# Optimization experiments

Hardware: AMD Instinct MI355X
Metric: run time of the kernel (lower is better)

Reference implementation:

```python
import jax, jax.numpy as jnp
import numpy as np

D_MODEL, H, KV, HD = 2048, 32, 8, 64  # head_dim = 64, RoPE half-dim = 32
B, L = 2, 2048
EPS = 1e-06


def apply_rope(t, cos, sin):
    # t: [b,l,h,hd]; cos/sin: [1,l,1,hd//2] (broadcast over batch and heads)
    dim = t.shape[-1] // 2
    cos = cos[..., :dim]
    sin = sin[..., :dim]
    x1, x2 = t[..., :dim], t[..., dim:]
    return jnp.concatenate([x1 * cos - x2 * sin, x2 * cos + x1 * sin], axis=-1)


def setup_inputs() -> dict:
    key = jax.random.key(0)
    ks = jax.random.split(key, 5)
    x = jax.random.normal(ks[0], (B, L, D_MODEL), dtype=jnp.float32)
    # true rotary tables, theta=10000
    half = HD // 2
    inv_freq = 1.0 / (10000.0 ** (jnp.arange(half, dtype=jnp.float32) / half))
    ang = jnp.arange(L, dtype=jnp.float32)[:, None] * inv_freq[None, :]  # [L, half]
    cos = jnp.cos(ang)[None, :, None, :]  # [1,L,1,half]
    sin = jnp.sin(ang)[None, :, None, :]
    s = 0.02
    Wq = jax.random.normal(ks[1], (D_MODEL, D_MODEL), dtype=jnp.float32) * s
    Wk = jax.random.normal(ks[2], (D_MODEL, KV * HD), dtype=jnp.float32) * s
    Wv = jax.random.normal(ks[3], (D_MODEL, KV * HD), dtype=jnp.float32) * s
    Wo = jax.random.normal(ks[4], (D_MODEL, D_MODEL), dtype=jnp.float32) * s
    return {"x": x, "cos": cos, "sin": sin, "Wq": Wq, "Wk": Wk, "Wv": Wv, "Wo": Wo}


def reference(x, cos, sin, Wq, Wk, Wv, Wo):
    b, l, _ = x.shape
    q = (x @ Wq).reshape(b, l, H, HD)
    k = (x @ Wk).reshape(b, l, KV, HD)
    v = (x @ Wv).reshape(b, l, KV, HD)
    q = apply_rope(q, cos, sin)
    k = apply_rope(k, cos[:, :, :KV, :], sin[:, :, :KV, :])
    # QK RMS-norm (qk_norm=True path), done in fp32
    q32 = q.astype(jnp.float32)
    k32 = k.astype(jnp.float32)
    q = (q32 * jax.lax.rsqrt(jnp.mean(jnp.square(q32), axis=-1, keepdims=True) + EPS)).astype(q.dtype)
    k = (k32 * jax.lax.rsqrt(jnp.mean(jnp.square(k32), axis=-1, keepdims=True) + EPS)).astype(k.dtype)
    # GQA: repeat KV heads to match Q heads
    g = H // KV
    k = jnp.repeat(k, g, axis=2)
    v = jnp.repeat(v, g, axis=2)
    scale = jax.lax.rsqrt(jnp.float32(HD))
    scores = jnp.einsum('blhd,bmhd->bhlm', q, k) * scale  # [b,H,L,L]
    causal = jnp.tril(jnp.ones((l, l), dtype=jnp.bool_))[None, None]
    scores = jnp.where(causal, scores, jnp.full_like(scores, -10000.0))
    attn = jax.nn.softmax(scores.astype(jnp.float32), axis=-1).astype(v.dtype)
    out = jnp.einsum('bhql,blhd->bqhd', attn, v).reshape(b, l, D_MODEL)
    return out @ Wo
```

## Files before the change

### kernel.cpp

```cpp
#include <hip/hip_runtime.h>
#include <hip/hip_bf16.h>
#include <cstdint>
#include <cstddef>

#define D_MODEL 2048
#define NH 32
#define NKV 8
#define HD 64
#define BB 2
#define LL 2048
#define EPS 1e-6f
#define MM (BB * LL)
#define QS 3072
#define KO 2048
#define VO 2560
#define QSCALE 0.18033688f

typedef __hip_bfloat16 bf16;
typedef short bf16x8 __attribute__((ext_vector_type(8)));
typedef short s16x4 __attribute__((ext_vector_type(4)));
typedef float f32x4 __attribute__((ext_vector_type(4)));

__device__ inline float4 ld_bf4u(const unsigned short* p) {
  const ushort4 u = *(const ushort4*)p;
  float4 r;
  r.x = __uint_as_float(((unsigned)u.x) << 16);
  r.y = __uint_as_float(((unsigned)u.y) << 16);
  r.z = __uint_as_float(((unsigned)u.z) << 16);
  r.w = __uint_as_float(((unsigned)u.w) << 16);
  return r;
}
__device__ inline float4 ld4_rt(const void* p, size_t i, bool f32) {
  if (f32) return *(const float4*)((const float*)p + i);
  return ld_bf4u((const unsigned short*)p + i);
}
__device__ inline float ld1_rt(const void* p, size_t i, bool f32) {
  if (f32) return ((const float*)p)[i];
  unsigned short u = ((const unsigned short*)p)[i];
  return __uint_as_float(((unsigned)u) << 16);
}
__device__ inline unsigned short f2bf(float f) {
  bf16 h = __float2bfloat16(f);
  return *reinterpret_cast<unsigned short*>(&h);
}
__device__ inline float bfu2f(unsigned short u) {
  return __uint_as_float(((unsigned)u) << 16);
}
__device__ inline void store1(float* p, float v) { *p = v; }
__device__ inline void store1(unsigned short* p, float v) { *p = f2bf(v); }

__device__ inline void glds16(const unsigned short* g, unsigned short* l) {
  __builtin_amdgcn_global_load_lds(
      (const __attribute__((address_space(1))) unsigned int*)g,
      (__attribute__((address_space(3))) unsigned int*)l, 16, 0, 0);
}

__global__ __launch_bounds__(256) void detect_all(
    const unsigned short* p0, const unsigned short* p1, const unsigned short* p2,
    const unsigned short* p3, const unsigned short* p4, const unsigned short* p5,
    const unsigned short* p6, int* __restrict__ flags) {
  const unsigned short* ptrs[7] = {p0, p1, p2, p3, p4, p5, p6};
  const int b = blockIdx.x;
  const uint4* p = (const uint4*)ptrs[b];
  __shared__ int found;
  if (threadIdx.x == 0) found = 0;
  __syncthreads();
  int loc = 0;
#pragma unroll
  for (int it = 0; it < 16; ++it) {
    uint4 v = p[it * 256 + threadIdx.x];
    unsigned wds[4] = {v.x, v.y, v.z, v.w};
#pragma unroll
    for (int q = 0; q < 4; ++q) {
      unsigned lo = wds[q] & 0xFFFFu, hi = wds[q] >> 16;
      if (((lo >> 7) & 0xFFu) == 0xFFu || ((hi >> 7) & 0xFFu) == 0xFFu) loc = 1;
    }
  }
  if (loc) atomicOr(&found, 1);
  __syncthreads();
  if (threadIdx.x == 0) flags[b] = found;
}

__global__ __launch_bounds__(256) void cvt_bf16(const void* __restrict__ src,
                                                unsigned short* __restrict__ dst,
                                                int n4, const int* __restrict__ flags, int idx) {
  const bool f32 = flags[idx] != 0;
  int i = blockIdx.x * 256 + threadIdx.x;
  if (i < n4) {
    float4 v = ld4_rt(src, (size_t)i * 4, f32);
    ushort4 o;
    o.x = f2bf(v.x); o.y = f2bf(v.y); o.z = f2bf(v.z); o.w = f2bf(v.w);
    *(ushort4*)&dst[(size_t)i * 4] = o;
  }
}

__global__ __launch_bounds__(256) void transpose_all(
    const void* __restrict__ Wq, const void* __restrict__ Wk,
    const void* __restrict__ Wv, const void* __restrict__ Wo,
    unsigned short* __restrict__ WqkvT, unsigned short* __restrict__ WoT,
    const int* __restrict__ flags) {
  const int z = blockIdx.z;
  const void* srcs[4] = {Wq, Wk, Wv, Wo};
  unsigned short* dsts[4] = {WqkvT, WqkvT + (size_t)KO * 2048, WqkvT + (size_t)VO * 2048, WoT};
  const int Ns[4] = {2048, 512, 512, 2048};
  const int N = Ns[z];
  if (blockIdx.x * 64 >= N) return;
  const void* src = srcs[z];
  unsigned short* dst = dsts[z];
  const bool f32 = flags[3 + z] != 0;
  const int K = 2048;
  __shared__ unsigned short tile[64][65];
  const int t = threadIdx.x;
  const int n0 = blockIdx.x * 64, k0 = blockIdx.y * 64;
  const int cr = t >> 4, cc = (t & 15) * 4;
#pragma unroll
  for (int rr = 0; rr < 4; ++rr) {
    int row = rr * 16 + cr;
    float4 v = ld4_rt(src, (size_t)(k0 + row) * N + n0 + cc, f32);
    tile[row][cc + 0] = f2bf(v.x);
    tile[row][cc + 1] = f2bf(v.y);
    tile[row][cc + 2] = f2bf(v.z);
    tile[row][cc + 3] = f2bf(v.w);
  }
  __syncthreads();
#pragma unroll
  for (int rr = 0; rr < 4; ++rr) {
    int nrow = rr * 16 + cr;
    ushort4 o;
    o.x = tile[cc + 0][nrow];
    o.y = tile[cc + 1][nrow];
    o.z = tile[cc + 2][nrow];
    o.w = tile[cc + 3][nrow];
    *(ushort4*)&dst[(size_t)(n0 + nrow) * K + k0 + cc] = o;
  }
}

template <typename CT, int FUSE>
__global__ __launch_bounds__(256) void gemm_mfma(const unsigned short* __restrict__ A,
                                                 const unsigned short* __restrict__ Bt,
                                                 CT* __restrict__ C,
                                                 int M, int N, int K, int lda,
                                                 const void* __restrict__ cosp,
                                                 const void* __restrict__ sinp,
                                                 const int* __restrict__ flags,
                                                 unsigned short* __restrict__ vt) {
  __shared__ __align__(16) unsigned short As[3][128 * 32];
  __shared__ __align__(16) unsigned short Bs[3][128 * 32];
  const int t = threadIdx.x;
  const int lane = t & 63, w = t >> 6;
  const int wm = (w >> 1) * 64, wn = (w & 1) * 64;
  const int g = lane >> 4, m16 = lane & 15;
  const int nwg = gridDim.x * gridDim.y;
  const int orig = blockIdx.y * gridDim.x + blockIdx.x;
  const int swz = (orig & 7) * (nwg >> 3) + (orig >> 3);
  const int m0 = (swz / gridDim.x) * 128, n0 = (swz % gridDim.x) * 128;
  const int csw = (t & 3) ^ ((t >> 3) & 3);
  const unsigned short* gA = &A[(size_t)(m0 + (t >> 2)) * lda + csw * 8];
  const unsigned short* gB = &Bt[(size_t)(n0 + (t >> 2)) * K + csw * 8];
  const int l8 = t * 8;
  const int cs8 = (g ^ ((m16 >> 1) & 3)) * 8;
  f32x4 acc[4][4] = {};
  const int T = K >> 5;

#define STAGE(k0_, buf_)                                        \
  do {                                                          \
    glds16(gA + (k0_), &As[buf_][l8]);                          \
    glds16(gA + (size_t)64 * lda + (k0_), &As[buf_][l8 + 2048]);\
    glds16(gB + (k0_), &Bs[buf_][l8]);                          \
    glds16(gB + (size_t)64 * K + (k0_), &Bs[buf_][l8 + 2048]);  \
  } while (0)

  STAGE(0, 0);
  STAGE(32, 1);
  asm volatile("s_waitcnt vmcnt(4)" ::: "memory");
  __builtin_amdgcn_s_barrier();

  int buf = 0;
  for (int tt = 0; tt < T; ++tt) {
    const int k0 = tt << 5;
    if (tt + 2 < T) {
      int nb = buf + 2; if (nb >= 3) nb -= 3;
      STAGE(k0 + 64, nb);
    }
    bf16x8 af[4], bfr[4];
#pragma unroll
    for (int i = 0; i < 4; ++i) af[i] = *(const bf16x8*)&As[buf][(wm + i * 16 + m16) * 32 + cs8];
#pragma unroll
    for (int j = 0; j < 4; ++j) bfr[j] = *(const bf16x8*)&Bs[buf][(wn + j * 16 + m16) * 32 + cs8];
#pragma unroll
    for (int i = 0; i < 4; ++i)
#pragma unroll
      for (int j = 0; j < 4; ++j)
        acc[i][j] = __builtin_amdgcn_mfma_f32_16x16x32_bf16(af[i], bfr[j], acc[i][j], 0, 0, 0);
    if (tt + 1 < T) {
      if (tt + 2 < T) asm volatile("s_waitcnt vmcnt(4)" ::: "memory");
      else            asm volatile("s_waitcnt vmcnt(0)" ::: "memory");
      __builtin_amdgcn_s_barrier();
    }
    ++buf; if (buf >= 3) buf = 0;
  }
#undef STAGE

  if constexpr (FUSE) {
    const int colbase = n0 + wn;
    if (colbase < VO) {
      const bool cf = flags[1] != 0, sf = flags[2] != 0;
      const float post = (colbase < KO) ? QSCALE : 1.0f;
#pragma unroll
      for (int i = 0; i < 4; ++i)
#pragma unroll
        for (int r = 0; r < 4; ++r) {
          const int row = m0 + wm + i * 16 + g * 4 + r;
          const int l = row & (LL - 1);
          const float c0 = ld1_rt(cosp, l * 32 + m16, cf);
          const float c1 = ld1_rt(cosp, l * 32 + 16 + m16, cf);
          const float s0 = ld1_rt(sinp, l * 32 + m16, sf);
          const float s1 = ld1_rt(sinp, l * 32 + 16 + m16, sf);
          const float x0 = acc[i][0][r], x1 = acc[i][1][r];
          const float x2 = acc[i][2][r], x3 = acc[i][3][r];
          const float r0 = x0 * c0 - x2 * s0;
          const float r1 = x1 * c1 - x3 * s1;
          const float r2 = x2 * c0 + x0 * s0;
          const float r3 = x3 * c1 + x1 * s1;
          float ss = r0 * r0 + r1 * r1 + r2 * r2 + r3 * r3;
#pragma unroll
          for (int off = 1; off < 16; off <<= 1) ss += __shfl_xor(ss, off);
          const float sc = rsqrtf(ss * (1.0f / HD) + EPS) * post;
          CT* cr = &C[(size_t)row * N + colbase + m16];
          store1(cr + 0, r0 * sc);
          store1(cr + 16, r1 * sc);
          store1(cr + 32, r2 * sc);
          store1(cr + 48, r3 * sc);
        }
    } else {
      const int bb = (m0 + wm) >> 11;
      const int lb = (m0 + wm) & (LL - 1);
      const int kvh = (colbase - VO) >> 6;
      unsigned short* vb = vt + (size_t)(bb * NKV + kvh) * 64 * LL;
#pragma unroll
      for (int j = 0; j < 4; ++j)
#pragma unroll
        for (int i = 0; i < 4; ++i) {
          ushort4 pw;
          pw.x = f2bf(acc[i][j][0]); pw.y = f2bf(acc[i][j][1]);
          pw.z = f2bf(acc[i][j][2]); pw.w = f2bf(acc[i][j][3]);
          *(ushort4*)&vb[(size_t)(j * 16 + m16) * LL + lb + i * 16 + g * 4] = pw;
        }
    }
    return;
  }
#pragma unroll
  for (int i = 0; i < 4; ++i)
#pragma unroll
    for (int j = 0; j < 4; ++j)
#pragma unroll
      for (int r = 0; r < 4; ++r) {
        int row = m0 + wm + i * 16 + g * 4 + r;
        int col = n0 + wn + j * 16 + m16;
        store1(&C[(size_t)row * N + col], acc[i][j][r]);
      }
}

__global__ __launch_bounds__(256) void attn_mfma(unsigned short* __restrict__ qkv,
                                                 const unsigned short* __restrict__ vt) {
  __shared__ __align__(16) unsigned short Ks[2][64 * 64];
  __shared__ __align__(16) unsigned short Vs[2][64 * 64];
  __shared__ __align__(16) unsigned short Pt[4][64 * 16];
  const int t = threadIdx.x, lane = t & 63, w = t >> 6;
  const int g = lane >> 4, m16 = lane & 15;
  const int h = blockIdx.x, b = blockIdx.y;
  const int qt = (LL / 64 - 1) - blockIdx.z;
  const int kvh = h >> 2;
  const int q0 = qt * 64, qr0 = q0 + w * 16;

  bf16x8 qf0, qf1;
  {
    const unsigned short* qrow = &qkv[(size_t)(b * LL + qr0 + m16) * QS + h * 64 + g * 8];
    qf0 = *(const bf16x8*)&qrow[0];
    qf1 = *(const bf16x8*)&qrow[32];
  }
  f32x4 Oacc[4] = {};
  f32x4 lacc = {0.f, 0.f, 0.f, 0.f};
  const short one_bf = (short)0x3F80;
  const bf16x8 ones = {one_bf, one_bf, one_bf, one_bf, one_bf, one_bf, one_bf, one_bf};

  const int lr = lane >> 3;
  const int lc = (lane & 7) ^ lr;
  const unsigned short* gK = &qkv[(size_t)(b * LL) * QS + KO + kvh * 64 + lc * 8];
  const unsigned short* gV = &vt[((size_t)(b * NKV + kvh) * 64 + w * 16 + lr) * LL + lc * 8];
  const int dbase = w * 1024 + lane * 8;
  const int nIter = q0 / 64 + 1;

#pragma unroll
  for (int c = 0; c < 2; ++c) {
    glds16(gK + (size_t)(w * 16 + c * 8 + lr) * QS, &Ks[0][dbase + c * 512]);
    glds16(gV + (size_t)c * 8 * LL, &Vs[0][dbase + c * 512]);
  }
  __syncthreads();

  const int sw8 = (m16 & 7) * 8;
  for (int it = 0; it < nIter; ++it) {
    const int j0 = it * 64;
    const int cur = it & 1;
    if (it + 1 < nIter) {
      const int nj = j0 + 64;
#pragma unroll
      for (int c = 0; c < 2; ++c) {
        glds16(gK + (size_t)(nj + w * 16 + c * 8 + lr) * QS, &Ks[cur ^ 1][dbase + c * 512]);
        glds16(gV + (size_t)c * 8 * LL + nj, &Vs[cur ^ 1][dbase + c * 512]);
      }
    }
    const unsigned short* KsB = Ks[cur];
    const unsigned short* VsB = Vs[cur];

    f32x4 S[4];
    __builtin_amdgcn_s_setprio(1);
#pragma unroll
    for (int jt = 0; jt < 4; ++jt) {
      const int rb = (jt * 16 + m16) * 64;
      bf16x8 kf0 = *(const bf16x8*)&KsB[rb + ((g * 8) ^ sw8)];
      bf16x8 kf1 = *(const bf16x8*)&KsB[rb + (((g + 4) * 8) ^ sw8)];
      f32x4 z = {0.f, 0.f, 0.f, 0.f};
      z = __builtin_amdgcn_mfma_f32_16x16x32_bf16(qf0, kf0, z, 0, 0, 0);
      S[jt] = __builtin_amdgcn_mfma_f32_16x16x32_bf16(qf1, kf1, z, 0, 0, 0);
    }
    __builtin_amdgcn_s_setprio(0);
    if (j0 == q0) {
#pragma unroll
      for (int jt = 0; jt < 4; ++jt)
#pragma unroll
        for (int r = 0; r < 4; ++r) {
          int col = q0 + jt * 16 + m16;
          int row = qr0 + g * 4 + r;
          float p = __builtin_amdgcn_exp2f(S[jt][r]);
          S[jt][r] = (col <= row) ? p : 0.f;
        }
    } else {
#pragma unroll
      for (int jt = 0; jt < 4; ++jt)
#pragma unroll
        for (int r = 0; r < 4; ++r)
          S[jt][r] = __builtin_amdgcn_exp2f(S[jt][r]);
    }
#pragma unroll
    for (int jt = 0; jt < 4; ++jt) {
      ushort4 pw;
      pw.x = f2bf(S[jt][0]); pw.y = f2bf(S[jt][1]);
      pw.z = f2bf(S[jt][2]); pw.w = f2bf(S[jt][3]);
      *(ushort4*)&Pt[w][(jt * 16 + m16) * 16 + g * 4] = pw;
    }
    s16x4 a0, a1, b0, b1;
    {
      __attribute__((address_space(3))) unsigned short* p3 =
          (__attribute__((address_space(3))) unsigned short*)&Pt[w][g * 128 + m16 * 4];
      unsigned paddr = (unsigned)(size_t)p3;
      asm volatile(
          "s_waitcnt lgkmcnt(0)\n\t"
          "ds_read_b64_tr_b16 %0, %4\n\t"
          "ds_read_b64_tr_b16 %1, %4 offset:128\n\t"
          "ds_read_b64_tr_b16 %2, %4 offset:1024\n\t"
          "ds_read_b64_tr_b16 %3, %4 offset:1152\n\t"
          "s_waitcnt lgkmcnt(0)"
          : "=&v"(a0), "=&v"(a1), "=&v"(b0), "=&v"(b1)
          : "v"(paddr)
          : "memory");
      __builtin_amdgcn_sched_barrier(0);
    }
    bf16x8 pf0 = __builtin_shufflevector(a0, a1, 0, 1, 2, 3, 4, 5, 6, 7);
    bf16x8 pf1 = __builtin_shufflevector(b0, b1, 0, 1, 2, 3, 4, 5, 6, 7);
    __builtin_amdgcn_s_setprio(1);
    lacc = __builtin_amdgcn_mfma_f32_16x16x32_bf16(pf0, ones, lacc, 0, 0, 0);
    lacc = __builtin_amdgcn_mfma_f32_16x16x32_bf16(pf1, ones, lacc, 0, 0, 0);
#pragma unroll
    for (int dt = 0; dt < 4; ++dt) {
      const int rb = (dt * 16 + m16) * 64;
      bf16x8 vf0 = *(const bf16x8*)&VsB[rb + ((g * 8) ^ sw8)];
      bf16x8 vf1 = *(const bf16x8*)&VsB[rb + (((g + 4) * 8) ^ sw8)];
      Oacc[dt] = __builtin_amdgcn_mfma_f32_16x16x32_bf16(pf0, vf0, Oacc[dt], 0, 0, 0);
      Oacc[dt] = __builtin_amdgcn_mfma_f32_16x16x32_bf16(pf1, vf1, Oacc[dt], 0, 0, 0);
    }
    __builtin_amdgcn_s_setprio(0);
    __syncthreads();
  }
  float inv[4];
#pragma unroll
  for (int r = 0; r < 4; ++r) inv[r] = 1.0f / lacc[r];
#pragma unroll
  for (int dt = 0; dt < 4; ++dt)
#pragma unroll
    for (int r = 0; r < 4; ++r) {
      int row = qr0 + g * 4 + r;
      qkv[(size_t)(b * LL + row) * QS + h * 64 + dt * 16 + m16] = f2bf(Oacc[dt][r] * inv[r]);
    }
}

extern "C" void kernel_launch(void* const* d_in, const int* in_sizes, int n_in,
                              void* d_out, int out_size, void* d_ws, size_t ws_size,
                              hipStream_t stream) {
  const void* x = d_in[0];
  const void* cosp = d_in[1];
  const void* sinp = d_in[2];
  const void* Wq = d_in[3];
  const void* Wk = d_in[4];
  const void* Wv = d_in[5];
  const void* Wo = d_in[6];
  float* out = (float*)d_out;

  char* w0 = (char*)d_ws;
  int* flags = (int*)w0;
  unsigned short* xb = (unsigned short*)(w0 + 256);
  unsigned short* qkvb = xb + (size_t)MM * 2048;
  unsigned short* WqkvT = qkvb + (size_t)MM * QS;
  unsigned short* WoT = WqkvT + (size_t)QS * 2048;
  unsigned short* vt = WoT + (size_t)2048 * 2048;

  detect_all<<<7, 256, 0, stream>>>(
      (const unsigned short*)x, (const unsigned short*)cosp, (const unsigned short*)sinp,
      (const unsigned short*)Wq, (const unsigned short*)Wk, (const unsigned short*)Wv,
      (const unsigned short*)Wo, flags);
  cvt_bf16<<<MM * 2048 / 4 / 256, 256, 0, stream>>>(x, xb, MM * 2048 / 4, flags, 0);
  transpose_all<<<dim3(32, 32, 4), 256, 0, stream>>>(Wq, Wk, Wv, Wo, WqkvT, WoT, flags);
  gemm_mfma<unsigned short, 1><<<dim3(QS / 128, MM / 128), 256, 0, stream>>>(
      xb, WqkvT, qkvb, MM, QS, 2048, 2048, cosp, sinp, flags, vt);
  attn_mfma<<<dim3(NH, BB, LL / 64), 256, 0, stream>>>(qkvb, vt);
  gemm_mfma<float, 0><<<dim3(2048 / 128, MM / 128), 256, 0, stream>>>(
      qkvb, WoT, out, MM, 2048, 2048, QS, nullptr, nullptr, nullptr, nullptr);
}
```

Baseline: 309.7 us.

## Use 128-row query tiles with 8 waves sharing K/V staging; merge prep kernels

Result: faster. 297.0 us (-4.1%).

```diff
diff --git a/kernel.cpp b/kernel.cpp
--- a/kernel.cpp
+++ b/kernel.cpp
@@ -81,37 +81,39 @@
   if (threadIdx.x == 0) flags[b] = found;
 }
 
-__global__ __launch_bounds__(256) void cvt_bf16(const void* __restrict__ src,
-                                                unsigned short* __restrict__ dst,
-                                                int n4, const int* __restrict__ flags, int idx) {
-  const bool f32 = flags[idx] != 0;
-  int i = blockIdx.x * 256 + threadIdx.x;
-  if (i < n4) {
-    float4 v = ld4_rt(src, (size_t)i * 4, f32);
-    ushort4 o;
-    o.x = f2bf(v.x); o.y = f2bf(v.y); o.z = f2bf(v.z); o.w = f2bf(v.w);
-    *(ushort4*)&dst[(size_t)i * 4] = o;
-  }
-}
-
-__global__ __launch_bounds__(256) void transpose_all(
+__global__ __launch_bounds__(256) void prep_all(
+    const void* __restrict__ x, unsigned short* __restrict__ xb,
     const void* __restrict__ Wq, const void* __restrict__ Wk,
     const void* __restrict__ Wv, const void* __restrict__ Wo,
     unsigned short* __restrict__ WqkvT, unsigned short* __restrict__ WoT,
     const int* __restrict__ flags) {
-  const int z = blockIdx.z;
+  const int bid = blockIdx.x;
+  const int t = threadIdx.x;
+  if (bid < 8192) {
+    const bool f32 = flags[0] != 0;
+    int i = bid * 256 + t;
+    float4 v = ld4_rt(x, (size_t)i * 4, f32);
+    ushort4 o;
+    o.x = f2bf(v.x); o.y = f2bf(v.y); o.z = f2bf(v.z); o.w = f2bf(v.w);
+    *(ushort4*)&xb[(size_t)i * 4] = o;
+    return;
+  }
+  int r = bid - 8192;
+  int z, bx, by;
+  if (r < 1024)      { z = 0; bx = r & 31; by = r >> 5; }
+  else if (r < 1280) { z = 1; r -= 1024; bx = r & 7; by = r >> 3; }
+  else if (r < 1536) { z = 2; r -= 1280; bx = r & 7; by = r >> 3; }
+  else               { z = 3; r -= 1536; bx = r & 31; by = r >> 5; }
   const void* srcs[4] = {Wq, Wk, Wv, Wo};
   unsigned short* dsts[4] = {WqkvT, WqkvT + (size_t)KO * 2048, WqkvT + (size_t)VO * 2048, WoT};
   const int Ns[4] = {2048, 512, 512, 2048};
   const int N = Ns[z];
-  if (blockIdx.x * 64 >= N) return;
   const void* src = srcs[z];
   unsigned short* dst = dsts[z];
   const bool f32 = flags[3 + z] != 0;
   const int K = 2048;
   __shared__ unsigned short tile[64][65];
-  const int t = threadIdx.x;
-  const int n0 = blockIdx.x * 64, k0 = blockIdx.y * 64;
+  const int n0 = bx * 64, k0 = by * 64;
   const int cr = t >> 4, cc = (t & 15) * 4;
 #pragma unroll
   for (int rr = 0; rr < 4; ++rr) {
@@ -261,17 +263,18 @@
       }
 }
 
-__global__ __launch_bounds__(256) void attn_mfma(unsigned short* __restrict__ qkv,
+__global__ __launch_bounds__(512) void attn_mfma(unsigned short* __restrict__ qkv,
                                                  const unsigned short* __restrict__ vt) {
   __shared__ __align__(16) unsigned short Ks[2][64 * 64];
   __shared__ __align__(16) unsigned short Vs[2][64 * 64];
-  __shared__ __align__(16) unsigned short Pt[4][64 * 16];
+  __shared__ __align__(16) unsigned short Pt[8][64 * 16];
   const int t = threadIdx.x, lane = t & 63, w = t >> 6;
   const int g = lane >> 4, m16 = lane & 15;
   const int h = blockIdx.x, b = blockIdx.y;
-  const int qt = (LL / 64 - 1) - blockIdx.z;
+  const int qt = (LL / 128 - 1) - blockIdx.z;
   const int kvh = h >> 2;
-  const int q0 = qt * 64, qr0 = q0 + w * 16;
+  const int q0 = qt * 128, qr0 = q0 + w * 16;
+  const int dtile = q0 + ((w >> 2) << 6);
 
   bf16x8 qf0, qf1;
   {
@@ -286,16 +289,13 @@
 
   const int lr = lane >> 3;
   const int lc = (lane & 7) ^ lr;
-  const unsigned short* gK = &qkv[(size_t)(b * LL) * QS + KO + kvh * 64 + lc * 8];
-  const unsigned short* gV = &vt[((size_t)(b * NKV + kvh) * 64 + w * 16 + lr) * LL + lc * 8];
-  const int dbase = w * 1024 + lane * 8;
-  const int nIter = q0 / 64 + 1;
-
-#pragma unroll
-  for (int c = 0; c < 2; ++c) {
-    glds16(gK + (size_t)(w * 16 + c * 8 + lr) * QS, &Ks[0][dbase + c * 512]);
-    glds16(gV + (size_t)c * 8 * LL, &Vs[0][dbase + c * 512]);
-  }
+  const unsigned short* gK = &qkv[(size_t)(b * LL + w * 8 + lr) * QS + KO + kvh * 64 + lc * 8];
+  const unsigned short* gV = &vt[((size_t)(b * NKV + kvh) * 64 + w * 8 + lr) * LL + lc * 8];
+  const int dbase = w * 512 + lane * 8;
+  const int nIter = q0 / 64 + 2;
+
+  glds16(gK, &Ks[0][dbase]);
+  glds16(gV, &Vs[0][dbase]);
   __syncthreads();
 
   const int sw8 = (m16 & 7) * 8;
@@ -304,82 +304,81 @@
     const int cur = it & 1;
     if (it + 1 < nIter) {
       const int nj = j0 + 64;
-#pragma unroll
-      for (int c = 0; c < 2; ++c) {
-        glds16(gK + (size_t)(nj + w * 16 + c * 8 + lr) * QS, &Ks[cur ^ 1][dbase + c * 512]);
-        glds16(gV + (size_t)c * 8 * LL + nj, &Vs[cur ^ 1][dbase + c * 512]);
-      }
-    }
-    const unsigned short* KsB = Ks[cur];
-    const unsigned short* VsB = Vs[cur];
-
-    f32x4 S[4];
-    __builtin_amdgcn_s_setprio(1);
-#pragma unroll
-    for (int jt = 0; jt < 4; ++jt) {
-      const int rb = (jt * 16 + m16) * 64;
-      bf16x8 kf0 = *(const bf16x8*)&KsB[rb + ((g * 8) ^ sw8)];
-      bf16x8 kf1 = *(const bf16x8*)&KsB[rb + (((g + 4) * 8) ^ sw8)];
-      f32x4 z = {0.f, 0.f, 0.f, 0.f};
-      z = __builtin_amdgcn_mfma_f32_16x16x32_bf16(qf0, kf0, z, 0, 0, 0);
-      S[jt] = __builtin_amdgcn_mfma_f32_16x16x32_bf16(qf1, kf1, z, 0, 0, 0);
-    }
-    __builtin_amdgcn_s_setprio(0);
-    if (j0 == q0) {
-#pragma unroll
-      for (int jt = 0; jt < 4; ++jt)
-#pragma unroll
-        for (int r = 0; r < 4; ++r) {
-          int col = q0 + jt * 16 + m16;
-          int row = qr0 + g * 4 + r;
-          float p = __builtin_amdgcn_exp2f(S[jt][r]);
-          S[jt][r] = (col <= row) ? p : 0.f;
-        }
-    } else {
-#pragma unroll
-      for (int jt = 0; jt < 4; ++jt)
-#pragma unroll
-        for (int r = 0; r < 4; ++r)
-          S[jt][r] = __builtin_amdgcn_exp2f(S[jt][r]);
-    }
-#pragma unroll
-    for (int jt = 0; jt < 4; ++jt) {
-      ushort4 pw;
-      pw.x = f2bf(S[jt][0]); pw.y = f2bf(S[jt][1]);
-      pw.z = f2bf(S[jt][2]); pw.w = f2bf(S[jt][3]);
-      *(ushort4*)&Pt[w][(jt * 16 + m16) * 16 + g * 4] = pw;
-    }
-    s16x4 a0, a1, b0, b1;
-    {
-      __attribute__((address_space(3))) unsigned short* p3 =
-          (__attribute__((address_space(3))) unsigned short*)&Pt[w][g * 128 + m16 * 4];
-      unsigned paddr = (unsigned)(size_t)p3;
-      asm volatile(
-          "s_waitcnt lgkmcnt(0)\n\t"
-          "ds_read_b64_tr_b16 %0, %4\n\t"
-          "ds_read_b64_tr_b16 %1, %4 offset:128\n\t"
-          "ds_read_b64_tr_b16 %2, %4 offset:1024\n\t"
-          "ds_read_b64_tr_b16 %3, %4 offset:1152\n\t"
-          "s_waitcnt lgkmcnt(0)"
-          : "=&v"(a0), "=&v"(a1), "=&v"(b0), "=&v"(b1)
-          : "v"(paddr)
-          : "memory");
-      __builtin_amdgcn_sched_barrier(0);
-    }
-    bf16x8 pf0 = __builtin_shufflevector(a0, a1, 0, 1, 2, 3, 4, 5, 6, 7);
-    bf16x8 pf1 = __builtin_shufflevector(b0, b1, 0, 1, 2, 3, 4, 5, 6, 7);
-    __builtin_amdgcn_s_setprio(1);
-    lacc = __builtin_amdgcn_mfma_f32_16x16x32_bf16(pf0, ones, lacc, 0, 0, 0);
-    lacc = __builtin_amdgcn_mfma_f32_16x16x32_bf16(pf1, ones, lacc, 0, 0, 0);
-#pragma unroll
-    for (int dt = 0; dt < 4; ++dt) {
-      const int rb = (dt * 16 + m16) * 64;
-      bf16x8 vf0 = *(const bf16x8*)&VsB[rb + ((g * 8) ^ sw8)];
-      bf16x8 vf1 = *(const bf16x8*)&VsB[rb + (((g + 4) * 8) ^ sw8)];
-      Oacc[dt] = __builtin_amdgcn_mfma_f32_16x16x32_bf16(pf0, vf0, Oacc[dt], 0, 0, 0);
-      Oacc[dt] = __builtin_amdgcn_mfma_f32_16x16x32_bf16(pf1, vf1, Oacc[dt], 0, 0, 0);
-    }
-    __builtin_amdgcn_s_setprio(0);
+      glds16(gK + (size_t)nj * QS, &Ks[cur ^ 1][dbase]);
+      glds16(gV + nj, &Vs[cur ^ 1][dbase]);
+    }
+    if (j0 <= dtile) {
+      const unsigned short* KsB = Ks[cur];
+      const unsigned short* VsB = Vs[cur];
+
+      f32x4 S[4];
+      __builtin_amdgcn_s_setprio(1);
+#pragma unroll
+      for (int jt = 0; jt < 4; ++jt) {
+        const int rb = (jt * 16 + m16) * 64;
+        bf16x8 kf0 = *(const bf16x8*)&KsB[rb + ((g * 8) ^ sw8)];
+        bf16x8 kf1 = *(const bf16x8*)&KsB[rb + (((g + 4) * 8) ^ sw8)];
+        f32x4 z = {0.f, 0.f, 0.f, 0.f};
+        z = __builtin_amdgcn_mfma_f32_16x16x32_bf16(qf0, kf0, z, 0, 0, 0);
+        S[jt] = __builtin_amdgcn_mfma_f32_16x16x32_bf16(qf1, kf1, z, 0, 0, 0);
+      }
+      __builtin_amdgcn_s_setprio(0);
+      if (j0 == dtile) {
+#pragma unroll
+        for (int jt = 0; jt < 4; ++jt)
+#pragma unroll
+          for (int r = 0; r < 4; ++r) {
+            int col = j0 + jt * 16 + m16;
+            int row = qr0 + g * 4 + r;
+            float p = __builtin_amdgcn_exp2f(S[jt][r]);
+            S[jt][r] = (col <= row) ? p : 0.f;
+          }
+      } else {
+#pragma unroll
+        for (int jt = 0; jt < 4; ++jt)
+#pragma unroll
+          for (int r = 0; r < 4; ++r)
+            S[jt][r] = __builtin_amdgcn_exp2f(S[jt][r]);
+      }
+#pragma unroll
+      for (int jt = 0; jt < 4; ++jt) {
+        ushort4 pw;
+        pw.x = f2bf(S[jt][0]); pw.y = f2bf(S[jt][1]);
+        pw.z = f2bf(S[jt][2]); pw.w = f2bf(S[jt][3]);
+        *(ushort4*)&Pt[w][(jt * 16 + m16) * 16 + g * 4] = pw;
+      }
+      s16x4 a0, a1, b0, b1;
+      {
+        __attribute__((address_space(3))) unsigned short* p3 =
+            (__attribute__((address_space(3))) unsigned short*)&Pt[w][g * 128 + m16 * 4];
+        unsigned paddr = (unsigned)(size_t)p3;
+        asm volatile(
+            "s_waitcnt lgkmcnt(0)\n\t"
+            "ds_read_b64_tr_b16 %0, %4\n\t"
+            "ds_read_b64_tr_b16 %1, %4 offset:128\n\t"
+            "ds_read_b64_tr_b16 %2, %4 offset:1024\n\t"
+            "ds_read_b64_tr_b16 %3, %4 offset:1152\n\t"
+            "s_waitcnt lgkmcnt(0)"
+            : "=&v"(a0), "=&v"(a1), "=&v"(b0), "=&v"(b1)
+            : "v"(paddr)
+            : "memory");
+        __builtin_amdgcn_sched_barrier(0);
+      }
+      bf16x8 pf0 = __builtin_shufflevector(a0, a1, 0, 1, 2, 3, 4, 5, 6, 7);
+      bf16x8 pf1 = __builtin_shufflevector(b0, b1, 0, 1, 2, 3, 4, 5, 6, 7);
+      __builtin_amdgcn_s_setprio(1);
+      lacc = __builtin_amdgcn_mfma_f32_16x16x32_bf16(pf0, ones, lacc, 0, 0, 0);
+      lacc = __builtin_amdgcn_mfma_f32_16x16x32_bf16(pf1, ones, lacc, 0, 0, 0);
+#pragma unroll
+      for (int dt = 0; dt < 4; ++dt) {
+        const int rb = (dt * 16 + m16) * 64;
+        bf16x8 vf0 = *(const bf16x8*)&VsB[rb + ((g * 8) ^ sw8)];
+        bf16x8 vf1 = *(const bf16x8*)&VsB[rb + (((g + 4) * 8) ^ sw8)];
+        Oacc[dt] = __builtin_amdgcn_mfma_f32_16x16x32_bf16(pf0, vf0, Oacc[dt], 0, 0, 0);
+        Oacc[dt] = __builtin_amdgcn_mfma_f32_16x16x32_bf16(pf1, vf1, Oacc[dt], 0, 0, 0);
+      }
+      __builtin_amdgcn_s_setprio(0);
+    }
     __syncthreads();
   }
   float inv[4];
@@ -418,11 +417,10 @@
       (const unsigned short*)x, (const unsigned short*)cosp, (const unsigned short*)sinp,
       (const unsigned short*)Wq, (const unsigned short*)Wk, (const unsigned short*)Wv,
       (const unsigned short*)Wo, flags);
-  cvt_bf16<<<MM * 2048 / 4 / 256, 256, 0, stream>>>(x, xb, MM * 2048 / 4, flags, 0);
-  transpose_all<<<dim3(32, 32, 4), 256, 0, stream>>>(Wq, Wk, Wv, Wo, WqkvT, WoT, flags);
+  prep_all<<<10752, 256, 0, stream>>>(x, xb, Wq, Wk, Wv, Wo, WqkvT, WoT, flags);
   gemm_mfma<unsigned short, 1><<<dim3(QS / 128, MM / 128), 256, 0, stream>>>(
       xb, WqkvT, qkvb, MM, QS, 2048, 2048, cosp, sinp, flags, vt);
-  attn_mfma<<<dim3(NH, BB, LL / 64), 256, 0, stream>>>(qkvb, vt);
+  attn_mfma<<<dim3(NH, BB, LL / 128), 512, 0, stream>>>(qkvb, vt);
   gemm_mfma<float, 0><<<dim3(2048 / 128, MM / 128), 256, 0, stream>>>(
       qkvb, WoT, out, MM, 2048, 2048, QS, nullptr, nullptr, nullptr, nullptr);
 }
```
